# Kernel tuning notes

Hardware: AMD Instinct MI355X
Metric: run time of the kernel (lower is better)

## Reference

```python
import jax, jax.numpy as jnp
import numpy as np

N = 10000   # total nodes (hits) across events
K = 16      # n_neighbours (excluding self)
F = 64      # input feature dim
H = 128     # hidden width (hard-coded in module)
BIG = 1e9

def _selu(x):
    return jax.nn.selu(x)

def _glorot(key, shape):
    fan_in, fan_out = shape
    s = jnp.sqrt(2.0 / (fan_in + fan_out)).astype(jnp.float32)
    return jax.random.normal(key, shape, dtype=jnp.float32) * s

def setup_inputs() -> dict:
    key = jax.random.key(0)
    ks = jax.random.split(key, 10)
    h = jax.random.normal(ks[0], (N, F), dtype=jnp.float32)
    coords = jax.random.normal(ks[1], (N, 3), dtype=jnp.float32)
    row_splits = jnp.array([0, N // 2, N], dtype=jnp.int32)
    return {
        'h': h, 'coords': coords, 'row_splits': row_splits,
        'W_e1': _glorot(ks[2], (2 * F + 1, H)), 'b_e1': jnp.zeros((H,), jnp.float32),
        'W_e2': _glorot(ks[3], (H, H)), 'b_e2': jnp.zeros((H,), jnp.float32),
        'W_c1': _glorot(ks[4], (H, H)), 'b_c1': jnp.zeros((H,), jnp.float32),
        'W_c2': _glorot(ks[5], (H, 1)), 'b_c2': jnp.zeros((1,), jnp.float32),
        'W_n1': _glorot(ks[6], (H + F, H)), 'b_n1': jnp.zeros((H,), jnp.float32),
        'W_n2': _glorot(ks[7], (H, H)), 'b_n2': jnp.zeros((H,), jnp.float32),
    }

def _knn(coords, row_splits):
    # segment id per node from row_splits (constant)
    n = coords.shape[0]
    seg = jnp.searchsorted(row_splits, jnp.arange(n), side='right') - 1
    nrm = jnp.sum(coords * coords, axis=1)                      # [N]
    d2 = nrm[:, None] + nrm[None, :] - 2.0 * (coords @ coords.T)
    d2 = jnp.maximum(d2, 0.0)
    same = seg[:, None] == seg[None, :]
    d2 = jnp.where(same, d2, BIG)
    negd, idx = jax.lax.top_k(-d2, K + 1)                       # includes self (dist 0)
    dist = jnp.maximum(-negd, 0.0)                              # [N, K+1]
    return idx, dist

def reference(h, coords, row_splits, W_e1, b_e1, W_e2, b_e2, W_c1, b_c1, W_c2, b_c2, W_n1, b_n1, W_n2, b_n2):
    idx, dist = _knn(coords, row_splits)                        # [N,K+1]
    nidx = idx[:, 1:]                                           # [N,K]
    d = dist[:, 1:]                                             # [N,K]
    coord_diff = coords[:, None, :] - coords[idx[:, 1:]]        # [N,K,3]

    hg = h[idx]                                                 # SelectWithDefault gather [N,K+1,F]
    h_self = hg[:, 0, :]                                        # [N,F]
    h_node = jnp.broadcast_to(h_self[:, None, :], (h.shape[0], K, F)).reshape(-1, F)
    h_neig = hg[:, 1:, :].reshape(-1, F)
    radial0 = d.reshape(-1, 1)

    e = jnp.concatenate([radial0, h_node, h_neig], axis=1)      # [N*K, 2F+1]
    e = _selu(e @ W_e1 + b_e1)
    e = _selu(e @ W_e2 + b_e2)                                  # [N*K, H]

    c = _selu(e @ W_c1 + b_c1)
    w = (c @ W_c2 + b_c2).reshape(-1, K, 1)                     # [N,K,1]
    trans = jnp.mean(coord_diff * w, axis=1)                    # [N,3]
    coords_new = coords + trans

    e_sum = e.reshape(-1, K, H).sum(axis=1)                     # [N,H]
    agg = jnp.concatenate([e_sum, h_self], axis=1)              # [N,H+F]
    out = _selu(agg @ W_n1 + b_n1) @ W_n2 + b_n2                # [N,H]
    return out, coords_new, nidx, d
```

## Files before the change

kernel.cpp:

```cpp
#include <hip/hip_runtime.h>
#include <cstdint>

#define KNB 16
#define FDIM 64
#define HDIM 128
#define NPB 8
#define ROWS 128
#define SA 136
#define SAD 68
#define SW 68
#define CMAXW 80

typedef unsigned long long ull;
typedef _Float16 f16x8 __attribute__((ext_vector_type(8)));
typedef float    f32x16 __attribute__((ext_vector_type(16)));

__device__ __forceinline__ float selu_f(float x){
    const float a = 1.6732632423543772f, s = 1.0507009873554805f;
    return x > 0.f ? s * x : s * a * (__expf(x) - 1.0f);
}

__device__ __forceinline__ unsigned int pack2(float a, float b){
    union { _Float16 h[2]; unsigned int u; } t;
    t.h[0] = (_Float16)a; t.h[1] = (_Float16)b;
    return t.u;
}

__device__ __forceinline__ f16x8 ldfrag4(const unsigned int* p, unsigned int di){
    union { uint4 q; f16x8 v; } t;
    t.q = *(const uint4*)(p + di);
    return t.v;
}

template<int CTRL>
__device__ __forceinline__ unsigned int dppmin_u32(unsigned int v){
    unsigned int t = (unsigned int)__builtin_amdgcn_update_dpp(
        -1, (int)v, CTRL, 0xF, 0xF, false);
    return t < v ? t : v;
}
__device__ __forceinline__ unsigned int wave_min_u32(unsigned int v){
    v = dppmin_u32<0x111>(v);
    v = dppmin_u32<0x112>(v);
    v = dppmin_u32<0x114>(v);
    v = dppmin_u32<0x118>(v);
    v = dppmin_u32<0x142>(v);
    v = dppmin_u32<0x143>(v);
    return (unsigned int)__builtin_amdgcn_readlane((int)v, 63);
}

__global__ __launch_bounds__(256) void conv_kernel(
    const float* __restrict__ We1, const float* __restrict__ We2,
    const float* __restrict__ Wc1, _Float16* __restrict__ WT)
{
    int id = blockIdx.x * 256 + threadIdx.x;
    int m  = id >> 14;
    int r  = id & 16383;
    int nn = (r >> 7) & 127;
    int k  = r & 127;
    float v;
    if (m == 0)      v = We1[(k + 1) * 128 + nn];
    else if (m == 1) v = We2[k * 128 + nn];
    else             v = Wc1[k * 128 + nn];
    WT[m * 16384 + nn * 128 + k] = (_Float16)v;
}

__global__ __launch_bounds__(256) void pack4_kernel(
    const float* __restrict__ coords, float4* __restrict__ c4, int n)
{
    int i = blockIdx.x * 256 + threadIdx.x;
    if (i < n){
        float x = coords[3*i], y = coords[3*i+1], z = coords[3*i+2];
        float nrm = __fadd_rn(__fadd_rn(__fmul_rn(x,x), __fmul_rn(y,y)), __fmul_rn(z,z));
        c4[i] = make_float4(x, y, z, nrm);
    }
}

__global__ __launch_bounds__(256) void knn_kernel(
    const float4* __restrict__ c4,
    const int* __restrict__ row_splits, int nseg, int n,
    int* __restrict__ nidx, float* __restrict__ ndist, int* __restrict__ idx0,
    float* __restrict__ out_nidx, float* __restrict__ out_d)
{
    const int lane = threadIdx.x & 63;
    const int wid  = threadIdx.x >> 6;
    const int i    = blockIdx.x * 4 + wid;
    if (i >= n) return;

    int lo = 0, hi = n;
    for (int s = 0; s < nseg; ++s){
        int a = row_splits[s], b = row_splits[s+1];
        if (i >= a && i < b){ lo = a; hi = b; }
    }

    const float4 ci = c4[i];
    const float cx = ci.x, cy = ci.y, cz = ci.z, nrmi = ci.w;

    const int jbase = lo + lane;
    const float FINF = __uint_as_float(0x7f800000u);

    ull m1 = ~0ull, m2 = ~0ull, m3 = ~0ull;

    #define D2_OF(v) __fsub_rn(__fadd_rn(nrmi, (v).w), __fmul_rn(2.0f, \
        __fadd_rn(__fadd_rn(__fmul_rn(cx,(v).x), __fmul_rn(cy,(v).y)), __fmul_rn(cz,(v).z))))
    #define INS(kk) { \
        ull n1 = (kk) < m1 ? (kk) : m1; \
        ull t1 = (kk) < m1 ? m1 : (kk); \
        ull n2 = t1 < m2 ? t1 : m2; \
        ull t2 = t1 < m2 ? m2 : t1; \
        ull n3 = t2 < m3 ? t2 : m3; \
        m1 = n1; m2 = n2; m3 = n3; }

    for (int c0 = 0; c0 < CMAXW; c0 += 4){
        int j0 = jbase + (c0+0)*64;
        int j1 = jbase + (c0+1)*64;
        int j2 = jbase + (c0+2)*64;
        int j3 = jbase + (c0+3)*64;
        float4 v0 = c4[min(j0, hi-1)];
        float4 v1 = c4[min(j1, hi-1)];
        float4 v2 = c4[min(j2, hi-1)];
        float4 v3 = c4[min(j3, hi-1)];
        float d0 = (j0 < hi) ? fmaxf(D2_OF(v0), 0.0f) : FINF;
        float d1 = (j1 < hi) ? fmaxf(D2_OF(v1), 0.0f) : FINF;
        float d2 = (j2 < hi) ? fmaxf(D2_OF(v2), 0.0f) : FINF;
        float d3 = (j3 < hi) ? fmaxf(D2_OF(v3), 0.0f) : FINF;
        ull k0 = (((ull)__float_as_uint(d0)) << 32) | (unsigned int)j0;
        ull k1 = (((ull)__float_as_uint(d1)) << 32) | (unsigned int)j1;
        ull k2 = (((ull)__float_as_uint(d2)) << 32) | (unsigned int)j2;
        ull k3 = (((ull)__float_as_uint(d3)) << 32) | (unsigned int)j3;
        INS(k0) INS(k1) INS(k2) INS(k3)
    }
    int vcnt = 3;

    for (int r = 0; r < KNB + 1; ++r){
        unsigned int h32 = (unsigned int)(m1 >> 32);
        unsigned int l32 = (unsigned int)m1;
        unsigned int wmd = wave_min_u32(h32);
        unsigned int jm  = (h32 == wmd) ? l32 : 0xFFFFFFFFu;
        unsigned int wmj = wave_min_u32(jm);

        bool own = (h32 == wmd) && (l32 == wmj);
        bool need = false;
        if (own){
            int   j  = (int)wmj;
            float dv = __uint_as_float(wmd);
            if (r == 0){
                idx0[i] = j;
            } else {
                int rr = r - 1;
                nidx[i*KNB + rr]     = j;
                ndist[i*KNB + rr]    = dv;
                out_nidx[i*KNB + rr] = (float)j;
                out_d[i*KNB + rr]    = dv;
            }
            m1 = m2; m2 = m3; m3 = ~0ull;
            need = (--vcnt == 0);
        }

        if (__ballot((int)need)){
            if (need){
                ull b = (((ull)wmd) << 32) | wmj;
                m1 = m2 = m3 = ~0ull;
                for (int c = 0; c < CMAXW; ++c){
                    int j = jbase + c*64;
                    float4 v = c4[min(j, hi-1)];
                    float dv = (j < hi) ? fmaxf(D2_OF(v), 0.0f) : FINF;
                    ull kk = (((ull)__float_as_uint(dv)) << 32) | (unsigned int)j;
                    kk = kk > b ? kk : ~0ull;
                    INS(kk)
                }
                vcnt = 3;
            }
        }
    }
    #undef INS
    #undef D2_OF
}

__global__ __launch_bounds__(256, 2) void egcn_node_kernel(
    const float* __restrict__ h, const float* __restrict__ coords,
    const int* __restrict__ nidx, const float* __restrict__ ndist,
    const int* __restrict__ idx0, const _Float16* __restrict__ WTg,
    const float* __restrict__ W_e1, const float* __restrict__ b_e1,
    const float* __restrict__ b_e2, const float* __restrict__ b_c1,
    const float* __restrict__ W_c2, const float* __restrict__ b_c2,
    float* __restrict__ aggout, float* __restrict__ out_coords, int n)
{
    __shared__ __attribute__((aligned(16))) _Float16 Act[ROWS * SA];
    __shared__ __attribute__((aligned(16))) unsigned int wt[ROWS * SW];
    __shared__ float agg[NPB][HDIM];
    __shared__ float dls[ROWS];
    __shared__ int   nb[ROWS];
    __shared__ int   j0s[NPB];
    __shared__ float wedge[ROWS];

    const int g0  = blockIdx.x * NPB;
    const int tid = threadIdx.x;
    const int lane = tid & 63, wid = tid >> 6;
    const int ln31 = lane & 31, grp = lane >> 5;
    const int rt  = wid;

    if (tid < ROWS){
        int e = min(g0*KNB + tid, n*KNB - 1);
        nb[tid]  = nidx[e];
        dls[tid] = ndist[e];
    }
    if (tid < NPB) j0s[tid] = idx0[min(g0 + tid, n - 1)];
    __syncthreads();

    unsigned int* actd = (unsigned int*)Act;

    {
        int r = tid >> 1, half = tid & 1;
        const float4* hs = (const float4*)(h + (size_t)j0s[r >> 4] * FDIM + half*32);
        const float4* hn = (const float4*)(h + (size_t)nb[r] * FDIM + half*32);
        unsigned int base = (unsigned int)r * SAD + half*16;
        uint4 buf[4];
        #pragma unroll
        for (int q = 0; q < 4; ++q){
            float4 a = hs[2*q], b = hs[2*q+1];
            buf[q].x = pack2(a.x,a.y); buf[q].y = pack2(a.z,a.w);
            buf[q].z = pack2(b.x,b.y); buf[q].w = pack2(b.z,b.w);
        }
        #pragma unroll
        for (int q = 0; q < 4; ++q) *(uint4*)(actd + base + 4*q) = buf[q];
        #pragma unroll
        for (int q = 0; q < 4; ++q){
            float4 a = hn[2*q], b = hn[2*q+1];
            buf[q].x = pack2(a.x,a.y); buf[q].y = pack2(a.z,a.w);
            buf[q].z = pack2(b.x,b.y); buf[q].w = pack2(b.z,b.w);
        }
        #pragma unroll
        for (int q = 0; q < 4; ++q) *(uint4*)(actd + base + 32 + 4*q) = buf[q];
    }
    auto stage_wt = [&](const _Float16* Wg){
        int nr = tid >> 1, half = tid & 1;
        const uint4* src = (const uint4*)(Wg + nr * 128 + half*64);
        uint4* dst = (uint4*)(wt + nr * SW + half*32);
        #pragma unroll
        for (int q = 0; q < 8; ++q) dst[q] = src[q];
    };
    stage_wt(WTg);
    __syncthreads();

    const unsigned int aBase = (unsigned int)(rt*32 + ln31) * SAD + grp*4;
    const unsigned int bB0   = (unsigned int)(ln31      ) * SW + grp*4;
    const unsigned int bB1   = (unsigned int)(32  + ln31) * SW + grp*4;
    const unsigned int bB2   = (unsigned int)(64  + ln31) * SW + grp*4;
    const unsigned int bB3   = (unsigned int)(96  + ln31) * SW + grp*4;

    auto gemm4 = [&](f32x16& A0, f32x16& A1, f32x16& A2, f32x16& A3){
        #pragma unroll
        for (int ks = 0; ks < 8; ++ks){
            const unsigned int off = ks * 8;
            f16x8 af = ldfrag4(actd, aBase + off);
            A0 = __builtin_amdgcn_mfma_f32_32x32x16_f16(af, ldfrag4(wt, bB0 + off), A0, 0, 0, 0);
            A1 = __builtin_amdgcn_mfma_f32_32x32x16_f16(af, ldfrag4(wt, bB1 + off), A1, 0, 0, 0);
            A2 = __builtin_amdgcn_mfma_f32_32x32x16_f16(af, ldfrag4(wt, bB2 + off), A2, 0, 0, 0);
            A3 = __builtin_amdgcn_mfma_f32_32x32x16_f16(af, ldfrag4(wt, bB3 + off), A3, 0, 0, 0);
        }
    };
    #define ROW_OF(reg) (rt*32 + ((reg)&3) + 8*((reg)>>2) + 4*grp)

    {
        float w00 = W_e1[ln31],      w01 = W_e1[32+ln31];
        float w02 = W_e1[64+ln31],   w03 = W_e1[96+ln31];
        float bz0 = b_e1[ln31],      bz1 = b_e1[32+ln31];
        float bz2 = b_e1[64+ln31],   bz3 = b_e1[96+ln31];
        f32x16 a0, a1, a2, a3;
        #pragma unroll
        for (int reg = 0; reg < 16; ++reg){
            float dv = dls[ROW_OF(reg)];
            a0[reg] = fmaf(dv, w00, bz0);
            a1[reg] = fmaf(dv, w01, bz1);
            a2[reg] = fmaf(dv, w02, bz2);
            a3[reg] = fmaf(dv, w03, bz3);
        }
        gemm4(a0, a1, a2, a3);
        __syncthreads();
        #pragma unroll
        for (int reg = 0; reg < 16; ++reg){
            int row = ROW_OF(reg);
            Act[row*SA + ln31]      = (_Float16)selu_f(a0[reg]);
            Act[row*SA + 32 + ln31] = (_Float16)selu_f(a1[reg]);
            Act[row*SA + 64 + ln31] = (_Float16)selu_f(a2[reg]);
            Act[row*SA + 96 + ln31] = (_Float16)selu_f(a3[reg]);
        }
        stage_wt(WTg + 16384);
        __syncthreads();
    }

    {
        float bz0 = b_e2[ln31],    bz1 = b_e2[32+ln31];
        float bz2 = b_e2[64+ln31], bz3 = b_e2[96+ln31];
        f32x16 a0, a1, a2, a3;
        #pragma unroll
        for (int reg = 0; reg < 16; ++reg){ a0[reg]=bz0; a1[reg]=bz1; a2[reg]=bz2; a3[reg]=bz3; }
        gemm4(a0, a1, a2, a3);
        __syncthreads();
        float e0[16], e1v[16], e2v[16], e3[16];
        float sl0=0.f, sh0=0.f, sl1=0.f, sh1=0.f, sl2=0.f, sh2=0.f, sl3=0.f, sh3=0.f;
        #pragma unroll
        for (int reg = 0; reg < 16; ++reg){
            e0[reg]=selu_f(a0[reg]); e1v[reg]=selu_f(a1[reg]);
            e2v[reg]=selu_f(a2[reg]); e3[reg]=selu_f(a3[reg]);
            if (reg < 8){ sl0+=e0[reg]; sl1+=e1v[reg]; sl2+=e2v[reg]; sl3+=e3[reg]; }
            else        { sh0+=e0[reg]; sh1+=e1v[reg]; sh2+=e2v[reg]; sh3+=e3[reg]; }
        }
        sl0 += __shfl_xor(sl0, 32, 64);  sh0 += __shfl_xor(sh0, 32, 64);
        sl1 += __shfl_xor(sl1, 32, 64);  sh1 += __shfl_xor(sh1, 32, 64);
        sl2 += __shfl_xor(sl2, 32, 64);  sh2 += __shfl_xor(sh2, 32, 64);
        sl3 += __shfl_xor(sl3, 32, 64);  sh3 += __shfl_xor(sh3, 32, 64);
        if (grp == 0){
            agg[rt*2+0][ln31]      = sl0;  agg[rt*2+1][ln31]      = sh0;
            agg[rt*2+0][32 + ln31] = sl1;  agg[rt*2+1][32 + ln31] = sh1;
            agg[rt*2+0][64 + ln31] = sl2;  agg[rt*2+1][64 + ln31] = sh2;
            agg[rt*2+0][96 + ln31] = sl3;  agg[rt*2+1][96 + ln31] = sh3;
        }
        #pragma unroll
        for (int reg = 0; reg < 16; ++reg){
            int row = ROW_OF(reg);
            Act[row*SA + ln31]      = (_Float16)e0[reg];
            Act[row*SA + 32 + ln31] = (_Float16)e1v[reg];
            Act[row*SA + 64 + ln31] = (_Float16)e2v[reg];
            Act[row*SA + 96 + ln31] = (_Float16)e3[reg];
        }
        stage_wt(WTg + 2*16384);
        __syncthreads();
    }

    {
        float bz0 = b_c1[ln31],    bz1 = b_c1[32+ln31];
        float bz2 = b_c1[64+ln31], bz3 = b_c1[96+ln31];
        f32x16 a0, a1, a2, a3;
        #pragma unroll
        for (int reg = 0; reg < 16; ++reg){ a0[reg]=bz0; a1[reg]=bz1; a2[reg]=bz2; a3[reg]=bz3; }
        gemm4(a0, a1, a2, a3);
        __syncthreads();
        float wc0 = W_c2[ln31],    wc1 = W_c2[32+ln31];
        float wc2 = W_c2[64+ln31], wc3 = W_c2[96+ln31];
        float bc2 = b_c2[0];
        float p[16];
        #pragma unroll
        for (int reg = 0; reg < 16; ++reg)
            p[reg] = selu_f(a0[reg])*wc0 + selu_f(a1[reg])*wc1
                   + selu_f(a2[reg])*wc2 + selu_f(a3[reg])*wc3;
        #pragma unroll
        for (int msk = 16; msk > 0; msk >>= 1){
            #pragma unroll
            for (int reg = 0; reg < 16; ++reg)
                p[reg] += __shfl_xor(p[reg], msk, 64);
        }
        if (ln31 == 0){
            #pragma unroll
            for (int reg = 0; reg < 16; ++reg)
                wedge[ROW_OF(reg)] = bc2 + p[reg];
        }
        __syncthreads();
    }

    if (tid < 3*NPB){
        int nd = tid / 3, c = tid - nd*3;
        int gi = min(g0 + nd, n - 1);
        float ci = coords[3*gi + c];
        float s = 0.f;
        #pragma unroll
        for (int k = 0; k < KNB; ++k){
            int e = nd*KNB + k;
            s += (ci - coords[3*nb[e] + c]) * wedge[e];
        }
        if (g0 + nd < n) out_coords[3*gi + c] = ci + s * (1.0f/KNB);
    }

    for (int s = tid; s < NPB*192; s += 256){
        int nd = s / 192, c = s - nd*192;
        if (g0 + nd < n){
            float v = (c < HDIM) ? agg[nd][c]
                                 : h[(size_t)j0s[nd]*FDIM + (c - HDIM)];
            aggout[(size_t)(g0 + nd)*192 + c] = v;
        }
    }
}

#define NMB 16
__global__ __launch_bounds__(256) void node_mlp_kernel(
    const float* __restrict__ aggin,
    const float* __restrict__ W_n1, const float* __restrict__ b_n1,
    const float* __restrict__ W_n2, const float* __restrict__ b_n2,
    float* __restrict__ out, int n)
{
    __shared__ __attribute__((aligned(16))) float sinT[192][20];
    __shared__ float part[2][NMB][HDIM];

    const int g0  = blockIdx.x * NMB;
    const int tid = threadIdx.x;
    const int o    = tid & 127;
    const int half = tid >> 7;

    for (int s = tid; s < NMB*192; s += 256){
        size_t gidx = (size_t)g0*192 + s;
        size_t lim  = (size_t)n*192 - 1;
        float v = aggin[gidx < lim ? gidx : lim];
        int nd = s / 192, in = s - nd*192;
        sinT[in][nd] = v;
    }
    __syncthreads();

    {
        float a[NMB];
        #pragma unroll
        for (int d = 0; d < NMB; ++d) a[d] = 0.f;
        int in0 = half * 96;
        for (int in = in0; in < in0 + 96; ++in){
            float w = W_n1[in*HDIM + o];
            const float4* sp = (const float4*)&sinT[in][0];
            float4 v0 = sp[0], v1 = sp[1], v2 = sp[2], v3 = sp[3];
            a[0]  = fmaf(v0.x, w, a[0]);  a[1]  = fmaf(v0.y, w, a[1]);
            a[2]  = fmaf(v0.z, w, a[2]);  a[3]  = fmaf(v0.w, w, a[3]);
            a[4]  = fmaf(v1.x, w, a[4]);  a[5]  = fmaf(v1.y, w, a[5]);
            a[6]  = fmaf(v1.z, w, a[6]);  a[7]  = fmaf(v1.w, w, a[7]);
            a[8]  = fmaf(v2.x, w, a[8]);  a[9]  = fmaf(v2.y, w, a[9]);
            a[10] = fmaf(v2.z, w, a[10]); a[11] = fmaf(v2.w, w, a[11]);
            a[12] = fmaf(v3.x, w, a[12]); a[13] = fmaf(v3.y, w, a[13]);
            a[14] = fmaf(v3.z, w, a[14]); a[15] = fmaf(v3.w, w, a[15]);
        }
        #pragma unroll
        for (int d = 0; d < NMB; ++d) part[half][d][o] = a[d];
    }
    __syncthreads();

    for (int s = tid; s < NMB*HDIM; s += 256){
        int nd = s >> 7, o2 = s & 127;
        sinT[o2][nd] = selu_f(part[0][nd][o2] + part[1][nd][o2] + b_n1[o2]);
    }
    __syncthreads();

    {
        float a[NMB];
        #pragma unroll
        for (int d = 0; d < NMB; ++d) a[d] = 0.f;
        int in0 = half * 64;
        for (int in = in0; in < in0 + 64; ++in){
            float w = W_n2[in*HDIM + o];
            const float4* sp = (const float4*)&sinT[in][0];
            float4 v0 = sp[0], v1 = sp[1], v2 = sp[2], v3 = sp[3];
            a[0]  = fmaf(v0.x, w, a[0]);  a[1]  = fmaf(v0.y, w, a[1]);
            a[2]  = fmaf(v0.z, w, a[2]);  a[3]  = fmaf(v0.w, w, a[3]);
            a[4]  = fmaf(v1.x, w, a[4]);  a[5]  = fmaf(v1.y, w, a[5]);
            a[6]  = fmaf(v1.z, w, a[6]);  a[7]  = fmaf(v1.w, w, a[7]);
            a[8]  = fmaf(v2.x, w, a[8]);  a[9]  = fmaf(v2.y, w, a[9]);
            a[10] = fmaf(v2.z, w, a[10]); a[11] = fmaf(v2.w, w, a[11]);
            a[12] = fmaf(v3.x, w, a[12]); a[13] = fmaf(v3.y, w, a[13]);
            a[14] = fmaf(v3.z, w, a[14]); a[15] = fmaf(v3.w, w, a[15]);
        }
        #pragma unroll
        for (int d = 0; d < NMB; ++d) part[half][d][o] = a[d];
    }
    __syncthreads();

    for (int s = tid; s < NMB*HDIM; s += 256){
        int nd = s >> 7, o2 = s & 127;
        if (g0 + nd < n)
            out[(size_t)(g0 + nd)*HDIM + o2] =
                part[0][nd][o2] + part[1][nd][o2] + b_n2[o2];
    }
}

extern "C" void kernel_launch(void* const* d_in, const int* in_sizes, int n_in,
                              void* d_out, int out_size, void* d_ws, size_t ws_size,
                              hipStream_t stream)
{
    const float* h          = (const float*)d_in[0];
    const float* coords     = (const float*)d_in[1];
    const int*   row_splits = (const int*)  d_in[2];
    const float* W_e1 = (const float*)d_in[3];
    const float* b_e1 = (const float*)d_in[4];
    const float* W_e2 = (const float*)d_in[5];
    const float* b_e2 = (const float*)d_in[6];
    const float* W_c1 = (const float*)d_in[7];
    const float* b_c1 = (const float*)d_in[8];
    const float* W_c2 = (const float*)d_in[9];
    const float* b_c2 = (const float*)d_in[10];
    const float* W_n1 = (const float*)d_in[11];
    const float* b_n1 = (const float*)d_in[12];
    const float* W_n2 = (const float*)d_in[13];
    const float* b_n2 = (const float*)d_in[14];

    const int n    = in_sizes[0] / FDIM;
    const int nseg = in_sizes[2] - 1;

    float* out        = (float*)d_out;
    float* out_coords = out + (size_t)n * HDIM;
    float* out_nidx   = out_coords + (size_t)n * 3;
    float* out_d      = out_nidx + (size_t)n * KNB;

    int*       nidx_i = (int*)d_ws;
    float*     ndist  = (float*)(nidx_i + (size_t)n * KNB);
    int*       idx0   = (int*)(ndist + (size_t)n * KNB);
    _Float16*  WT     = (_Float16*)(idx0 + (size_t)n);
    float*     aggbuf = (float*)(WT + 3 * 16384);
    float4*    c4     = (float4*)(aggbuf + (size_t)n * 192);

    conv_kernel<<<192, 256, 0, stream>>>(W_e1, W_e2, W_c1, WT);
    pack4_kernel<<<(n + 255) / 256, 256, 0, stream>>>(coords, c4, n);

    knn_kernel<<<(n + 3) / 4, 256, 0, stream>>>(c4, row_splits, nseg, n,
                                                nidx_i, ndist, idx0, out_nidx, out_d);

    egcn_node_kernel<<<(n + NPB - 1) / NPB, 256, 0, stream>>>(
        h, coords, nidx_i, ndist, idx0, WT,
        W_e1, b_e1, b_e2, b_c1, W_c2, b_c2,
        aggbuf, out_coords, n);

    node_mlp_kernel<<<(n + NMB - 1) / NMB, 256, 0, stream>>>(
        aggbuf, W_n1, b_n1, W_n2, b_n2, out, n);
}
```

Baseline: 257.7 us.

## Fuse prep kernels, pad coords buffer, widen KNN loads, swizzle LDS tiles

Merges the weight-transpose and coordinate-pack kernels into one launch. The packed coordinate buffer is padded with sentinel entries so the KNN kernel can drop the min() clamp on its gather indices. The KNN scan now issues eight loads per iteration instead of four, giving more memory-level parallelism. The EGCN kernel replaces padded LDS row strides with an XOR swizzle to avoid bank conflicts while using less shared memory. The padding relies on segments never reading more than PADN entries past n, and the workspace must be large enough to hold it.

```diff
diff --git a/kernel.cpp b/kernel.cpp
--- a/kernel.cpp
+++ b/kernel.cpp
@@ -6,10 +6,8 @@
 #define HDIM 128
 #define NPB 8
 #define ROWS 128
-#define SA 136
-#define SAD 68
-#define SW 68
 #define CMAXW 80
+#define PADN 5120
 
 typedef unsigned long long ull;
 typedef _Float16 f16x8 __attribute__((ext_vector_type(8)));
@@ -48,30 +46,32 @@
     return (unsigned int)__builtin_amdgcn_readlane((int)v, 63);
 }
 
-__global__ __launch_bounds__(256) void conv_kernel(
+__global__ __launch_bounds__(256) void prep_kernel(
     const float* __restrict__ We1, const float* __restrict__ We2,
-    const float* __restrict__ Wc1, _Float16* __restrict__ WT)
+    const float* __restrict__ Wc1, _Float16* __restrict__ WT,
+    const float* __restrict__ coords, float4* __restrict__ c4, int n, int npad)
 {
-    int id = blockIdx.x * 256 + threadIdx.x;
-    int m  = id >> 14;
-    int r  = id & 16383;
-    int nn = (r >> 7) & 127;
-    int k  = r & 127;
-    float v;
-    if (m == 0)      v = We1[(k + 1) * 128 + nn];
-    else if (m == 1) v = We2[k * 128 + nn];
-    else             v = Wc1[k * 128 + nn];
-    WT[m * 16384 + nn * 128 + k] = (_Float16)v;
-}
-
-__global__ __launch_bounds__(256) void pack4_kernel(
-    const float* __restrict__ coords, float4* __restrict__ c4, int n)
-{
-    int i = blockIdx.x * 256 + threadIdx.x;
-    if (i < n){
-        float x = coords[3*i], y = coords[3*i+1], z = coords[3*i+2];
-        float nrm = __fadd_rn(__fadd_rn(__fmul_rn(x,x), __fmul_rn(y,y)), __fmul_rn(z,z));
-        c4[i] = make_float4(x, y, z, nrm);
+    int b = blockIdx.x;
+    if (b < 192){
+        int id = b * 256 + threadIdx.x;
+        int m  = id >> 14;
+        int r  = id & 16383;
+        int nn = (r >> 7) & 127;
+        int k  = r & 127;
+        float v;
+        if (m == 0)      v = We1[(k + 1) * 128 + nn];
+        else if (m == 1) v = We2[k * 128 + nn];
+        else             v = Wc1[k * 128 + nn];
+        WT[m * 16384 + nn * 128 + k] = (_Float16)v;
+    } else {
+        int i = (b - 192) * 256 + threadIdx.x;
+        if (i < n){
+            float x = coords[3*i], y = coords[3*i+1], z = coords[3*i+2];
+            float nrm = __fadd_rn(__fadd_rn(__fmul_rn(x,x), __fmul_rn(y,y)), __fmul_rn(z,z));
+            c4[i] = make_float4(x, y, z, nrm);
+        } else if (i < npad){
+            c4[i] = make_float4(0.f, 0.f, 0.f, __uint_as_float(0x7f800000u));
+        }
     }
 }
 
@@ -110,24 +110,19 @@
         ull n3 = t2 < m3 ? t2 : m3; \
         m1 = n1; m2 = n2; m3 = n3; }
 
-    for (int c0 = 0; c0 < CMAXW; c0 += 4){
-        int j0 = jbase + (c0+0)*64;
-        int j1 = jbase + (c0+1)*64;
-        int j2 = jbase + (c0+2)*64;
-        int j3 = jbase + (c0+3)*64;
-        float4 v0 = c4[min(j0, hi-1)];
-        float4 v1 = c4[min(j1, hi-1)];
-        float4 v2 = c4[min(j2, hi-1)];
-        float4 v3 = c4[min(j3, hi-1)];
-        float d0 = (j0 < hi) ? fmaxf(D2_OF(v0), 0.0f) : FINF;
-        float d1 = (j1 < hi) ? fmaxf(D2_OF(v1), 0.0f) : FINF;
-        float d2 = (j2 < hi) ? fmaxf(D2_OF(v2), 0.0f) : FINF;
-        float d3 = (j3 < hi) ? fmaxf(D2_OF(v3), 0.0f) : FINF;
-        ull k0 = (((ull)__float_as_uint(d0)) << 32) | (unsigned int)j0;
-        ull k1 = (((ull)__float_as_uint(d1)) << 32) | (unsigned int)j1;
-        ull k2 = (((ull)__float_as_uint(d2)) << 32) | (unsigned int)j2;
-        ull k3 = (((ull)__float_as_uint(d3)) << 32) | (unsigned int)j3;
-        INS(k0) INS(k1) INS(k2) INS(k3)
+    for (int c0 = 0; c0 < CMAXW; c0 += 8){
+        float4 v[8]; int jj[8];
+        #pragma unroll
+        for (int q = 0; q < 8; ++q){
+            jj[q] = jbase + (c0 + q)*64;
+            v[q]  = c4[jj[q]];
+        }
+        #pragma unroll
+        for (int q = 0; q < 8; ++q){
+            float dv = (jj[q] < hi) ? fmaxf(D2_OF(v[q]), 0.0f) : FINF;
+            ull kk = (((ull)__float_as_uint(dv)) << 32) | (unsigned int)jj[q];
+            INS(kk)
+        }
     }
     int vcnt = 3;
 
@@ -162,7 +157,7 @@
                 m1 = m2 = m3 = ~0ull;
                 for (int c = 0; c < CMAXW; ++c){
                     int j = jbase + c*64;
-                    float4 v = c4[min(j, hi-1)];
+                    float4 v = c4[j];
                     float dv = (j < hi) ? fmaxf(D2_OF(v), 0.0f) : FINF;
                     ull kk = (((ull)__float_as_uint(dv)) << 32) | (unsigned int)j;
                     kk = kk > b ? kk : ~0ull;
@@ -175,6 +170,8 @@
     #undef INS
     #undef D2_OF
 }
+
+#define SWZ(row, d) ((unsigned int)(d) ^ ((((unsigned int)(row)) & 7u) << 2))
 
 __global__ __launch_bounds__(256, 2) void egcn_node_kernel(
     const float* __restrict__ h, const float* __restrict__ coords,
@@ -185,8 +182,8 @@
     const float* __restrict__ W_c2, const float* __restrict__ b_c2,
     float* __restrict__ aggout, float* __restrict__ out_coords, int n)
 {
-    __shared__ __attribute__((aligned(16))) _Float16 Act[ROWS * SA];
-    __shared__ __attribute__((aligned(16))) unsigned int wt[ROWS * SW];
+    __shared__ __attribute__((aligned(16))) _Float16 Act[ROWS * 128];
+    __shared__ __attribute__((aligned(16))) unsigned int wt[ROWS * 64];
     __shared__ float agg[NPB][HDIM];
     __shared__ float dls[ROWS];
     __shared__ int   nb[ROWS];
@@ -213,7 +210,7 @@
         int r = tid >> 1, half = tid & 1;
         const float4* hs = (const float4*)(h + (size_t)j0s[r >> 4] * FDIM + half*32);
         const float4* hn = (const float4*)(h + (size_t)nb[r] * FDIM + half*32);
-        unsigned int base = (unsigned int)r * SAD + half*16;
+        unsigned int rb = (unsigned int)r * 64;
         uint4 buf[4];
         #pragma unroll
         for (int q = 0; q < 4; ++q){
@@ -222,7 +219,8 @@
             buf[q].z = pack2(b.x,b.y); buf[q].w = pack2(b.z,b.w);
         }
         #pragma unroll
-        for (int q = 0; q < 4; ++q) *(uint4*)(actd + base + 4*q) = buf[q];
+        for (int q = 0; q < 4; ++q)
+            *(uint4*)(actd + rb + SWZ(r, half*16 + 4*q)) = buf[q];
         #pragma unroll
         for (int q = 0; q < 4; ++q){
             float4 a = hn[2*q], b = hn[2*q+1];
@@ -230,36 +228,44 @@
             buf[q].z = pack2(b.x,b.y); buf[q].w = pack2(b.z,b.w);
         }
         #pragma unroll
-        for (int q = 0; q < 4; ++q) *(uint4*)(actd + base + 32 + 4*q) = buf[q];
+        for (int q = 0; q < 4; ++q)
+            *(uint4*)(actd + rb + SWZ(r, 32 + half*16 + 4*q)) = buf[q];
     }
     auto stage_wt = [&](const _Float16* Wg){
         int nr = tid >> 1, half = tid & 1;
         const uint4* src = (const uint4*)(Wg + nr * 128 + half*64);
-        uint4* dst = (uint4*)(wt + nr * SW + half*32);
-        #pragma unroll
-        for (int q = 0; q < 8; ++q) dst[q] = src[q];
+        unsigned int rb = (unsigned int)nr * 64;
+        #pragma unroll
+        for (int q = 0; q < 8; ++q)
+            *(uint4*)(wt + rb + SWZ(nr, half*32 + q*4)) = src[q];
     };
     stage_wt(WTg);
     __syncthreads();
 
-    const unsigned int aBase = (unsigned int)(rt*32 + ln31) * SAD + grp*4;
-    const unsigned int bB0   = (unsigned int)(ln31      ) * SW + grp*4;
-    const unsigned int bB1   = (unsigned int)(32  + ln31) * SW + grp*4;
-    const unsigned int bB2   = (unsigned int)(64  + ln31) * SW + grp*4;
-    const unsigned int bB3   = (unsigned int)(96  + ln31) * SW + grp*4;
+    const unsigned int sA    = ((unsigned int)ln31 & 7u) << 2;
+    const unsigned int aRow  = (unsigned int)(rt*32 + ln31) * 64;
+    const unsigned int bRow0 = (unsigned int)(ln31      ) * 64;
+    const unsigned int bRow1 = (unsigned int)(32  + ln31) * 64;
+    const unsigned int bRow2 = (unsigned int)(64  + ln31) * 64;
+    const unsigned int bRow3 = (unsigned int)(96  + ln31) * 64;
 
     auto gemm4 = [&](f32x16& A0, f32x16& A1, f32x16& A2, f32x16& A3){
         #pragma unroll
         for (int ks = 0; ks < 8; ++ks){
-            const unsigned int off = ks * 8;
-            f16x8 af = ldfrag4(actd, aBase + off);
-            A0 = __builtin_amdgcn_mfma_f32_32x32x16_f16(af, ldfrag4(wt, bB0 + off), A0, 0, 0, 0);
-            A1 = __builtin_amdgcn_mfma_f32_32x32x16_f16(af, ldfrag4(wt, bB1 + off), A1, 0, 0, 0);
-            A2 = __builtin_amdgcn_mfma_f32_32x32x16_f16(af, ldfrag4(wt, bB2 + off), A2, 0, 0, 0);
-            A3 = __builtin_amdgcn_mfma_f32_32x32x16_f16(af, ldfrag4(wt, bB3 + off), A3, 0, 0, 0);
+            const unsigned int o = ((unsigned int)(ks*8 + grp*4)) ^ sA;
+            f16x8 af = ldfrag4(actd, aRow + o);
+            A0 = __builtin_amdgcn_mfma_f32_32x32x16_f16(af, ldfrag4(wt, bRow0 + o), A0, 0, 0, 0);
+            A1 = __builtin_amdgcn_mfma_f32_32x32x16_f16(af, ldfrag4(wt, bRow1 + o), A1, 0, 0, 0);
+            A2 = __builtin_amdgcn_mfma_f32_32x32x16_f16(af, ldfrag4(wt, bRow2 + o), A2, 0, 0, 0);
+            A3 = __builtin_amdgcn_mfma_f32_32x32x16_f16(af, ldfrag4(wt, bRow3 + o), A3, 0, 0, 0);
         }
     };
     #define ROW_OF(reg) (rt*32 + ((reg)&3) + 8*((reg)>>2) + 4*grp)
+
+    auto act_st = [&](int row, int col, float v){
+        unsigned int d = SWZ(row, col >> 1);
+        Act[row*128 + (d << 1) + (col & 1)] = (_Float16)v;
+    };
 
     {
         float w00 = W_e1[ln31],      w01 = W_e1[32+ln31];
@@ -280,10 +286,10 @@
         #pragma unroll
         for (int reg = 0; reg < 16; ++reg){
             int row = ROW_OF(reg);
-            Act[row*SA + ln31]      = (_Float16)selu_f(a0[reg]);
-            Act[row*SA + 32 + ln31] = (_Float16)selu_f(a1[reg]);
-            Act[row*SA + 64 + ln31] = (_Float16)selu_f(a2[reg]);
-            Act[row*SA + 96 + ln31] = (_Float16)selu_f(a3[reg]);
+            act_st(row, ln31,      selu_f(a0[reg]));
+            act_st(row, 32 + ln31, selu_f(a1[reg]));
+            act_st(row, 64 + ln31, selu_f(a2[reg]));
+            act_st(row, 96 + ln31, selu_f(a3[reg]));
         }
         stage_wt(WTg + 16384);
         __syncthreads();
@@ -319,10 +325,10 @@
         #pragma unroll
         for (int reg = 0; reg < 16; ++reg){
             int row = ROW_OF(reg);
-            Act[row*SA + ln31]      = (_Float16)e0[reg];
-            Act[row*SA + 32 + ln31] = (_Float16)e1v[reg];
-            Act[row*SA + 64 + ln31] = (_Float16)e2v[reg];
-            Act[row*SA + 96 + ln31] = (_Float16)e3[reg];
+            act_st(row, ln31,      e0[reg]);
+            act_st(row, 32 + ln31, e1v[reg]);
+            act_st(row, 64 + ln31, e2v[reg]);
+            act_st(row, 96 + ln31, e3[reg]);
         }
         stage_wt(WTg + 2*16384);
         __syncthreads();
@@ -487,6 +493,7 @@
 
     const int n    = in_sizes[0] / FDIM;
     const int nseg = in_sizes[2] - 1;
+    const int npad = n + PADN;
 
     float* out        = (float*)d_out;
     float* out_coords = out + (size_t)n * HDIM;
@@ -500,8 +507,9 @@
     float*     aggbuf = (float*)(WT + 3 * 16384);
     float4*    c4     = (float4*)(aggbuf + (size_t)n * 192);
 
-    conv_kernel<<<192, 256, 0, stream>>>(W_e1, W_e2, W_c1, WT);
-    pack4_kernel<<<(n + 255) / 256, 256, 0, stream>>>(coords, c4, n);
+    const int prep_blocks = 192 + (npad + 255) / 256;
+    prep_kernel<<<prep_blocks, 256, 0, stream>>>(W_e1, W_e2, W_c1, WT,
+                                                 coords, c4, n, npad);
 
     knn_kernel<<<(n + 3) / 4, 256, 0, stream>>>(c4, row_splits, nseg, n,
                                                 nidx_i, ndist, idx0, out_nidx, out_d);
```

Measured after the change: 258.9 us. Within noise of the previous version (+0.5%).
